# Optimization experiments

Hardware: AMD Instinct MI355X
Metric: run time of the kernel (lower is better)

The kernel has to match this reference:

```python
import jax, jax.numpy as jnp
import numpy as np

BETA = 0.4
EPS = 0.05
NUM_CLASSES = 5


def _model_single(xi, W1, b1, W2, b2):
    # xi: [C, L] single sample -> logits [num_classes]
    h = jnp.tanh(xi.reshape(-1) @ W1 + b1)
    return h @ W2 + b2


def setup_inputs() -> dict:
    key = jax.random.key(0)
    k1, k2, k3, k4 = jax.random.split(key, 4)
    B, C, L, H = 8192, 1, 2048, 1024
    x = jax.random.normal(k1, (B, C, L), dtype=jnp.float32)
    y = jax.random.randint(k2, (B,), 0, NUM_CLASSES)
    W1 = jax.random.normal(k3, (C * L, H), dtype=jnp.float32) * (1.0 / np.sqrt(C * L).astype(np.float32))
    b1 = jnp.zeros((H,), dtype=jnp.float32)
    W2 = jax.random.normal(k4, (H, NUM_CLASSES), dtype=jnp.float32) * (1.0 / np.sqrt(H).astype(np.float32))
    b2 = jnp.zeros((NUM_CLASSES,), dtype=jnp.float32)
    return {"x": x, "y": y, "W1": W1, "b1": b1, "W2": W2, "b2": b2}


def reference(x, y, W1, b1, W2, b2):
    B = x.shape[0]
    # batched model forward (same math the torch loop calls per-sample)
    logits = jnp.tanh(x.reshape(B, -1) @ W1 + b1) @ W2 + b2  # [B, num_classes]

    y_onehot = jax.nn.one_hot(y, NUM_CLASSES, dtype=logits.dtype)
    mse_loss = jnp.mean((logits - y_onehot) ** 2)

    idx = jnp.arange(B)
    z_y = logits[idx, y]  # [B]
    margins = jnp.maximum(1.0 - z_y[:, None] + logits, 0.0)
    margins = margins.at[idx, y].set(0.0)
    margin_loss = margins.sum() / B

    # per-sample L1 norm of d z_y / d x_i: one batched vmap(grad) instead of a python loop
    def z_of_x(xi, yi):
        return _model_single(xi, W1, b1, W2, b2)[yi]

    grads = jax.vmap(jax.grad(z_of_x), in_axes=(0, 0))(x, y)  # [B, C, L]
    w_l1 = jnp.sum(jnp.abs(grads), axis=(1, 2))  # [B]

    R = w_l1 * EPS / (jnp.abs(z_y) + 1e-8)
    nsr_loss = BETA * jnp.mean(jnp.log1p(R))

    correct_mask = jnp.mean((jnp.argmax(logits, axis=1) == y).astype(logits.dtype))
    total_loss = mse_loss + (margin_loss + nsr_loss) * correct_mask
    return total_loss
```

## Files before the change

### kernel.cpp

```cpp
#include <hip/hip_runtime.h>
#include <hip/hip_bf16.h>
#include <hip/hip_fp8.h>

typedef unsigned short ushort_t;
typedef unsigned char uchar_t;
typedef __attribute__((ext_vector_type(8))) short short8;
typedef __attribute__((ext_vector_type(8))) unsigned short u16x8;
typedef __attribute__((ext_vector_type(4))) float f32x4;

#define BETA 0.4f
#define EPS_C 0.05f
#define NB 8192
#define NH 1024
#define NL 2048
#define NC 5
#define VSCALE 64.0f

static __device__ __forceinline__ float b2f(unsigned short u) {
    union { unsigned int i; float f; } x; x.i = ((unsigned int)u) << 16; return x.f;
}
static __device__ __forceinline__ unsigned short f2b(float f) {
    union { float f; unsigned int i; } x; x.f = f;
    unsigned int i = x.i;
    unsigned int r = (i + 0x7FFFu + ((i >> 16) & 1u)) >> 16;
    return (unsigned short)r;
}
static __device__ __forceinline__ uchar_t f2fp8(float f) {
    __hip_fp8_e4m3 t(f);
    return (uchar_t)t.__x;
}

static __device__ __forceinline__ void gload16(const ushort_t* g, ushort_t* l) {
    __builtin_amdgcn_global_load_lds((const __attribute__((address_space(1))) void*)g,
                                     (__attribute__((address_space(3))) void*)l, 16, 0, 0);
}
static __device__ __forceinline__ void gload16b(const uchar_t* g, uchar_t* l) {
    __builtin_amdgcn_global_load_lds((const __attribute__((address_space(1))) void*)g,
                                     (__attribute__((address_space(3))) void*)l, 16, 0, 0);
}

#define CFENCE() asm volatile("" ::: "memory")
#define MFMA16(d, a, b) __builtin_amdgcn_mfma_f32_16x16x32_bf16(a, b, d, 0, 0, 0)
#define MFMA8(d, a, b)  __builtin_amdgcn_mfma_f32_16x16x32_fp8_fp8(a, b, d, 0, 0, 0)

__global__ __launch_bounds__(256) void cvt_kernel(const float* __restrict__ in,
                                                  ushort_t* __restrict__ out, long n) {
    long i = ((long)blockIdx.x * 256 + threadIdx.x) * 8;
    if (i >= n) return;
    const float4 a = *(const float4*)(in + i);
    const float4 b = *(const float4*)(in + i + 4);
    u16x8 o;
    o[0] = f2b(a.x); o[1] = f2b(a.y); o[2] = f2b(a.z); o[3] = f2b(a.w);
    o[4] = f2b(b.x); o[5] = f2b(b.y); o[6] = f2b(b.z); o[7] = f2b(b.w);
    *(u16x8*)(out + i) = o;
}

__global__ __launch_bounds__(256) void trans_kernel(const float* __restrict__ W1,
                                                    ushort_t* __restrict__ W1Tb,
                                                    uchar_t* __restrict__ W1f8) {
    __shared__ float tile[32][33];
    const int tx = threadIdx.x & 31, ty = threadIdx.x >> 5;
    const int k0 = blockIdx.x * 32, n0 = blockIdx.y * 32;
#pragma unroll
    for (int i = 0; i < 4; ++i) {
        const float v = W1[(size_t)(k0 + ty + i * 8) * NH + n0 + tx];
        tile[ty + i * 8][tx] = v;
        W1f8[(size_t)(k0 + ty + i * 8) * NH + n0 + tx] = f2fp8(v * VSCALE);
    }
    __syncthreads();
#pragma unroll
    for (int i = 0; i < 4; ++i)
        W1Tb[(size_t)(n0 + ty + i * 8) * NL + k0 + tx] = f2b(tile[tx][ty + i * 8]);
}

__global__ __launch_bounds__(256, 2) void g128_1(const ushort_t* __restrict__ A,
                                                 const ushort_t* __restrict__ Bt,
                                                 const float* __restrict__ b1,
                                                 ushort_t* __restrict__ hout) {
    constexpr int K  = 2048;
    constexpr int NT = K / 64;

    __shared__ ushort_t As[2][8192];
    __shared__ ushort_t Bs[2][8192];

    const int tid = threadIdx.x;
    const int wv = tid >> 6, lane = tid & 63;
    const int wm = (wv >> 1) & 1, wn = wv & 1;
    const int fr = lane & 15, fg = lane >> 4;

    const int xcd = blockIdx.x & 7, loc = blockIdx.x >> 3;
    const int bm0 = (xcd * 8 + (loc >> 3)) * 128;
    const int bn0 = (loc & 7) * 128;

    const int srow = lane >> 3;
    const int scol = ((lane & 7) ^ srow) << 3;

#define STA(BUF, KT) {                                                      \
    _Pragma("unroll") for (int c_ = 0; c_ < 4; ++c_) {                      \
        const int row_ = c_ * 32 + wv * 8 + srow;                           \
        gload16(A + (size_t)(bm0 + row_) * K + (KT) * 64 + scol,            \
                &As[BUF][c_ * 2048 + wv * 512]);                            \
    } }
#define STB(BUF, KT) {                                                      \
    _Pragma("unroll") for (int c_ = 0; c_ < 4; ++c_) {                      \
        const int row_ = c_ * 32 + wv * 8 + srow;                           \
        gload16(Bt + (size_t)(bn0 + row_) * K + (KT) * 64 + scol,           \
                &Bs[BUF][c_ * 2048 + wv * 512]);                            \
    } }

    auto ldA = [&](int buf, int mf, int ks) -> short8 {
        const int row = wm * 64 + mf * 16 + fr;
        const int slot = ((ks << 2) + fg) ^ (row & 7);
        return *(const short8*)&As[buf][row * 64 + slot * 8];
    };
    auto ldB = [&](int buf, int nf, int ks) -> short8 {
        const int row = wn * 64 + nf * 16 + fr;
        const int slot = ((ks << 2) + fg) ^ (row & 7);
        return *(const short8*)&Bs[buf][row * 64 + slot * 8];
    };

    f32x4 acc[4][4] = {};

    STA(0, 0) STB(0, 0)
    asm volatile("s_waitcnt vmcnt(0)" ::: "memory");
    CFENCE(); __builtin_amdgcn_s_barrier(); CFENCE();

#define TILE(BUF, TT) {                                                     \
    const int t_ = (TT);                                                    \
    short8 af[4][2], bf[4][2];                                              \
    _Pragma("unroll") for (int n_ = 0; n_ < 4; ++n_) {                      \
        bf[n_][0] = ldB(BUF, n_, 0); bf[n_][1] = ldB(BUF, n_, 1);           \
    }                                                                       \
    _Pragma("unroll") for (int m_ = 0; m_ < 4; ++m_) {                      \
        af[m_][0] = ldA(BUF, m_, 0); af[m_][1] = ldA(BUF, m_, 1);           \
    }                                                                       \
    if (t_ + 1 < NT) { STA(BUF ^ 1, t_ + 1) STB(BUF ^ 1, t_ + 1) }          \
    CFENCE(); __builtin_amdgcn_s_barrier(); CFENCE();                       \
    __builtin_amdgcn_s_setprio(1);                                          \
    _Pragma("unroll") for (int m_ = 0; m_ < 4; ++m_)                        \
        _Pragma("unroll") for (int n_ = 0; n_ < 4; ++n_) {                  \
            acc[m_][n_] = MFMA16(acc[m_][n_], af[m_][0], bf[n_][0]);        \
            acc[m_][n_] = MFMA16(acc[m_][n_], af[m_][1], bf[n_][1]);        \
        }                                                                   \
    __builtin_amdgcn_s_setprio(0);                                          \
    asm volatile("s_waitcnt vmcnt(0)" ::: "memory");                        \
    CFENCE(); __builtin_amdgcn_s_barrier(); CFENCE();                       \
    }

#pragma unroll 1
    for (int t = 0; t < NT; t += 2) {
        TILE(0, t)
        TILE(1, t + 1)
    }
#undef TILE
#undef STA
#undef STB

#pragma unroll
    for (int m = 0; m < 4; ++m)
#pragma unroll
        for (int n = 0; n < 4; ++n) {
            const int col = bn0 + wn * 64 + n * 16 + fr;
            const float bb = b1[col];
            const size_t rbase = (size_t)(bm0 + wm * 64 + m * 16 + fg * 4) * NH + col;
#pragma unroll
            for (int r = 0; r < 4; ++r)
                hout[rbase + (size_t)r * NH] = f2b(tanhf(acc[m][n][r] + bb));
        }
}

__global__ __launch_bounds__(256, 4) void g2f8(const uchar_t* __restrict__ A,
                                               const uchar_t* __restrict__ Bt,
                                               float* __restrict__ partout) {
    constexpr int K  = 1024;
    constexpr int NT = K / 64;

    __shared__ uchar_t As[2][8192];
    __shared__ uchar_t Bs[2][8192];

    const int tid = threadIdx.x;
    const int wv = tid >> 6, lane = tid & 63;
    const int wm = (wv >> 1) & 1, wn = wv & 1;
    const int fr = lane & 15, fg = lane >> 4;

    const int xcd = blockIdx.x & 7, loc = blockIdx.x >> 3;
    const int bm0 = (xcd * 8 + (loc >> 4)) * 128;
    const int bnIdx = loc & 15;
    const int bn0 = bnIdx * 128;

    const int t8 = tid >> 3, t7 = tid & 7;

#define STAF(BUF, KT) {                                                     \
    _Pragma("unroll") for (int j_ = 0; j_ < 2; ++j_) {                      \
        const int r1_ = j_ * 32 + t8;                                       \
        const int sl_ = (t7 * 2) ^ ((r1_ & 7) << 1);                        \
        const int row_ = 2 * r1_ + (sl_ >> 3);                              \
        const int cb_ = (KT) * 64 + (sl_ & 7) * 8;                          \
        gload16b(A + (size_t)(bm0 + row_) * K + cb_,                        \
                 &As[BUF][j_ * 4096 + wv * 1024]);                          \
    } }
#define STBF(BUF, KT) {                                                     \
    _Pragma("unroll") for (int j_ = 0; j_ < 2; ++j_) {                      \
        const int r1_ = j_ * 32 + t8;                                       \
        const int sl_ = (t7 * 2) ^ ((r1_ & 7) << 1);                        \
        const int row_ = 2 * r1_ + (sl_ >> 3);                              \
        const int cb_ = (KT) * 64 + (sl_ & 7) * 8;                          \
        gload16b(Bt + (size_t)(bn0 + row_) * K + cb_,                       \
                 &Bs[BUF][j_ * 4096 + wv * 1024]);                          \
    } }

    auto ldA = [&](int buf, int mf, int ks) -> long {
        const int row = wm * 64 + mf * 16 + fr;
        const int r1 = row >> 1;
        const int phys = (((row & 1) << 3) | (ks << 2) | fg) ^ ((r1 & 7) << 1);
        return *(const long*)&As[buf][r1 * 128 + phys * 8];
    };
    auto ldB = [&](int buf, int nf, int ks) -> long {
        const int row = wn * 64 + nf * 16 + fr;
        const int r1 = row >> 1;
        const int phys = (((row & 1) << 3) | (ks << 2) | fg) ^ ((r1 & 7) << 1);
        return *(const long*)&Bs[buf][r1 * 128 + phys * 8];
    };

    f32x4 acc[4][4] = {};

    STAF(0, 0) STBF(0, 0)
    asm volatile("s_waitcnt vmcnt(0)" ::: "memory");
    CFENCE(); __builtin_amdgcn_s_barrier(); CFENCE();

#define TILEF(BUF, TT) {                                                    \
    const int t_ = (TT);                                                    \
    long af[4][2], bf[4][2];                                                \
    _Pragma("unroll") for (int n_ = 0; n_ < 4; ++n_) {                      \
        bf[n_][0] = ldB(BUF, n_, 0); bf[n_][1] = ldB(BUF, n_, 1);           \
    }                                                                       \
    _Pragma("unroll") for (int m_ = 0; m_ < 4; ++m_) {                      \
        af[m_][0] = ldA(BUF, m_, 0); af[m_][1] = ldA(BUF, m_, 1);           \
    }                                                                       \
    if (t_ + 1 < NT) { STAF(BUF ^ 1, t_ + 1) STBF(BUF ^ 1, t_ + 1) }        \
    CFENCE(); __builtin_amdgcn_s_barrier(); CFENCE();                       \
    __builtin_amdgcn_s_setprio(1);                                          \
    _Pragma("unroll") for (int m_ = 0; m_ < 4; ++m_)                        \
        _Pragma("unroll") for (int n_ = 0; n_ < 4; ++n_) {                  \
            acc[m_][n_] = MFMA8(acc[m_][n_], af[m_][0], bf[n_][0]);         \
            acc[m_][n_] = MFMA8(acc[m_][n_], af[m_][1], bf[n_][1]);         \
        }                                                                   \
    __builtin_amdgcn_s_setprio(0);                                          \
    asm volatile("s_waitcnt vmcnt(0)" ::: "memory");                        \
    CFENCE(); __builtin_amdgcn_s_barrier(); CFENCE();                       \
    }

#pragma unroll 1
    for (int t = 0; t < NT; t += 2) {
        TILEF(0, t)
        TILEF(1, t + 1)
    }
#undef TILEF
#undef STAF
#undef STBF

    __syncthreads();
    float* rsum = (float*)&As[0][0];
#pragma unroll
    for (int m = 0; m < 4; ++m)
#pragma unroll
        for (int r = 0; r < 4; ++r) {
            float s = 0.f;
#pragma unroll
            for (int n = 0; n < 4; ++n) s += fabsf(acc[m][n][r]);
            s += __shfl_xor(s, 1); s += __shfl_xor(s, 2);
            s += __shfl_xor(s, 4); s += __shfl_xor(s, 8);
            if (fr == 0) rsum[wn * 128 + wm * 64 + m * 16 + fg * 4 + r] = s;
        }
    __syncthreads();
    if (tid < 128)
        partout[(size_t)bnIdx * NB + bm0 + tid] = rsum[tid] + rsum[128 + tid];
}

__global__ __launch_bounds__(256) void rows_kernel(const ushort_t* __restrict__ hb,
                                                   const int* __restrict__ y,
                                                   const float* __restrict__ W2,
                                                   const float* __restrict__ b2,
                                                   uchar_t* __restrict__ vb,
                                                   float4* __restrict__ rowstats) {
    __shared__ float w2t[NC][NH];
    __shared__ float b2s[NC];
    const int tid = threadIdx.x;
    for (int i = tid; i < NH * NC; i += 256) w2t[i % NC][i / NC] = W2[i];
    if (tid < NC) b2s[tid] = b2[tid];
    __syncthreads();
    const int wid = tid >> 6, lane = tid & 63;
    const int row = blockIdx.x * 4 + wid;
    const ushort_t* hrow = hb + (size_t)row * NH;
    uchar_t* vrow = vb + (size_t)row * NH;
    const int yi = y[row];
    float d0 = 0, d1 = 0, d2 = 0, d3 = 0, d4 = 0;
#pragma unroll
    for (int it = 0; it < 2; ++it) {
        const int n0 = it * 512 + lane * 8;
        u16x8 hv = *(const u16x8*)(hrow + n0);
        float hh[8];
#pragma unroll
        for (int j = 0; j < 8; ++j) hh[j] = b2f(hv[j]);
#pragma unroll
        for (int c = 0; c < NC; ++c) {
            const float4 a = *(const float4*)&w2t[c][n0];
            const float4 b = *(const float4*)&w2t[c][n0 + 4];
            float d = hh[0] * a.x; d += hh[1] * a.y; d += hh[2] * a.z; d += hh[3] * a.w;
            d += hh[4] * b.x; d += hh[5] * b.y; d += hh[6] * b.z; d += hh[7] * b.w;
            if (c == 0) d0 += d; else if (c == 1) d1 += d; else if (c == 2) d2 += d;
            else if (c == 3) d3 += d; else d4 += d;
        }
        const float4 ya = *(const float4*)&w2t[yi][n0];
        const float4 yb = *(const float4*)&w2t[yi][n0 + 4];
        const float yw[8] = { ya.x, ya.y, ya.z, ya.w, yb.x, yb.y, yb.z, yb.w };
        union { uchar_t b[8]; long l; } ov;
#pragma unroll
        for (int j = 0; j < 8; ++j)
            ov.b[j] = f2fp8((1.f - hh[j] * hh[j]) * yw[j] * VSCALE);
        *(long*)(vrow + n0) = ov.l;
    }
#pragma unroll
    for (int off = 32; off; off >>= 1) {
        d0 += __shfl_xor(d0, off); d1 += __shfl_xor(d1, off); d2 += __shfl_xor(d2, off);
        d3 += __shfl_xor(d3, off); d4 += __shfl_xor(d4, off);
    }
    if (lane == 0) {
        float lg[NC] = { d0 + b2s[0], d1 + b2s[1], d2 + b2s[2], d3 + b2s[3], d4 + b2s[4] };
        float zy = lg[yi];
        float mse = 0.f, marg = 0.f;
        int amax = 0; float best = lg[0];
#pragma unroll
        for (int c = 0; c < NC; ++c) {
            float t = lg[c] - (c == yi ? 1.f : 0.f);
            mse += t * t;
            if (c != yi) marg += fmaxf(1.f - zy + lg[c], 0.f);
            if (lg[c] > best) { best = lg[c]; amax = c; }
        }
        rowstats[row] = make_float4(zy, mse, marg, (amax == yi) ? 1.f : 0.f);
    }
}

__global__ __launch_bounds__(256) void reduce_rows(const float4* __restrict__ rs,
                                                   const float* __restrict__ part,
                                                   int NT, float4* __restrict__ bsums) {
    const int tid = threadIdx.x;
    const int r = blockIdx.x * 256 + tid;
    float4 v = rs[r];
    float wl1 = 0.f;
    for (int t = 0; t < NT; ++t) wl1 += part[(size_t)t * NB + r];
    wl1 *= (1.0f / (VSCALE * VSCALE));
    float R = wl1 * EPS_C / (fabsf(v.x) + 1e-8f);
    float4 s = make_float4(v.y, v.z, v.w, log1pf(R));
#pragma unroll
    for (int off = 32; off; off >>= 1) {
        s.x += __shfl_down(s.x, off); s.y += __shfl_down(s.y, off);
        s.z += __shfl_down(s.z, off); s.w += __shfl_down(s.w, off);
    }
    __shared__ float4 red[4];
    if ((tid & 63) == 0) red[tid >> 6] = s;
    __syncthreads();
    if (tid == 0) {
        float4 t = red[0];
        for (int i = 1; i < 4; ++i) { t.x += red[i].x; t.y += red[i].y; t.z += red[i].z; t.w += red[i].w; }
        bsums[blockIdx.x] = t;
    }
}

__global__ void final_combine(const float4* __restrict__ bsums, int nb, float* __restrict__ out) {
    const int l = threadIdx.x;
    float4 s = (l < nb) ? bsums[l] : make_float4(0.f, 0.f, 0.f, 0.f);
#pragma unroll
    for (int off = 32; off; off >>= 1) {
        s.x += __shfl_down(s.x, off); s.y += __shfl_down(s.y, off);
        s.z += __shfl_down(s.z, off); s.w += __shfl_down(s.w, off);
    }
    if (l == 0) {
        const float Bf = (float)NB;
        out[0] = s.x / (Bf * (float)NC) + (s.y / Bf + BETA * s.w / Bf) * (s.z / Bf);
    }
}

extern "C" void kernel_launch(void* const* d_in, const int* in_sizes, int n_in,
                              void* d_out, int out_size, void* d_ws, size_t ws_size,
                              hipStream_t stream) {
    const float* x  = (const float*)d_in[0];
    const int*   y  = (const int*)d_in[1];
    const float* W1 = (const float*)d_in[2];
    const float* b1 = (const float*)d_in[3];
    const float* W2 = (const float*)d_in[4];
    const float* b2 = (const float*)d_in[5];
    float* out = (float*)d_out;

    char* ws = (char*)d_ws;
    ushort_t* W1Tb = (ushort_t*)(ws);
    uchar_t*  W1f8 = (uchar_t*)(ws + (4ul << 20));
    ushort_t* xb   = (ushort_t*)(ws + (8ul << 20));
    ushort_t* hb   = (ushort_t*)(ws + (40ul << 20));
    uchar_t*  vf8  = (uchar_t*)(ws + (56ul << 20));
    float4*   rowstats = (float4*)(ws + (72ul << 20));
    float*    part = (float*)(ws + (72ul << 20) + (1ul << 20));
    float4*   bsums = (float4*)(ws + (74ul << 20));

    cvt_kernel<<<(NB * (long)NL) / (256 * 8), 256, 0, stream>>>(x, xb, (long)NB * NL);
    trans_kernel<<<dim3(NL / 32, NH / 32), 256, 0, stream>>>(W1, W1Tb, W1f8);

    g128_1<<<512, 256, 0, stream>>>(xb, W1Tb, b1, hb);

    rows_kernel<<<NB / 4, 256, 0, stream>>>(hb, y, W2, b2, vf8, rowstats);

    g2f8<<<1024, 256, 0, stream>>>(vf8, W1f8, part);

    reduce_rows<<<NB / 256, 256, 0, stream>>>(rowstats, part, NL / 128, bsums);
    final_combine<<<1, 64, 0, stream>>>(bsums, NB / 256, out);
}
```

Baseline: 113.0 us.

## Restructure first GEMM to two waves per block with 128x64 warp tiles

The bf16 x·W1 GEMM now runs 128-thread blocks (2 waves), each wave computing a full 128x64 output tile with 8x4 MFMA accumulators. The K step shrinks from 64 to 32, and the LDS layout packs two 32-wide rows per 64-element line with an XOR swizzle. The aim is more MFMA work per LDS fragment load and less shared memory per block. The cost is doubled accumulator registers, fewer waves per CU, and twice as many barrier iterations over K.

```diff
diff --git a/kernel.cpp b/kernel.cpp
--- a/kernel.cpp
+++ b/kernel.cpp
@@ -73,53 +73,60 @@
         W1Tb[(size_t)(n0 + ty + i * 8) * NL + k0 + tx] = f2b(tile[tx][ty + i * 8]);
 }
 
-__global__ __launch_bounds__(256, 2) void g128_1(const ushort_t* __restrict__ A,
-                                                 const ushort_t* __restrict__ Bt,
-                                                 const float* __restrict__ b1,
-                                                 ushort_t* __restrict__ hout) {
+__global__ __launch_bounds__(128, 2) void g128_2w(const ushort_t* __restrict__ A,
+                                                  const ushort_t* __restrict__ Bt,
+                                                  const float* __restrict__ b1,
+                                                  ushort_t* __restrict__ hout) {
     constexpr int K  = 2048;
-    constexpr int NT = K / 64;
-
-    __shared__ ushort_t As[2][8192];
-    __shared__ ushort_t Bs[2][8192];
+    constexpr int NT = K / 32;
+
+    __shared__ ushort_t As[2][4096];
+    __shared__ ushort_t Bs[2][4096];
 
     const int tid = threadIdx.x;
     const int wv = tid >> 6, lane = tid & 63;
-    const int wm = (wv >> 1) & 1, wn = wv & 1;
+    const int wn = wv;
     const int fr = lane & 15, fg = lane >> 4;
 
     const int xcd = blockIdx.x & 7, loc = blockIdx.x >> 3;
     const int bm0 = (xcd * 8 + (loc >> 3)) * 128;
     const int bn0 = (loc & 7) * 128;
 
-    const int srow = lane >> 3;
-    const int scol = ((lane & 7) ^ srow) << 3;
+    const int t8 = tid >> 3, t7 = tid & 7;
 
 #define STA(BUF, KT) {                                                      \
-    _Pragma("unroll") for (int c_ = 0; c_ < 4; ++c_) {                      \
-        const int row_ = c_ * 32 + wv * 8 + srow;                           \
-        gload16(A + (size_t)(bm0 + row_) * K + (KT) * 64 + scol,            \
-                &As[BUF][c_ * 2048 + wv * 512]);                            \
+    _Pragma("unroll") for (int j_ = 0; j_ < 4; ++j_) {                      \
+        const int r1_ = j_ * 16 + t8;                                       \
+        const int sl_ = t7 ^ (r1_ & 7);                                     \
+        const int row_ = 2 * r1_ + (sl_ >> 2);                              \
+        const int col_ = (KT) * 32 + (sl_ & 3) * 8;                         \
+        gload16(A + (size_t)(bm0 + row_) * K + col_,                        \
+                &As[BUF][j_ * 1024 + wv * 512]);                            \
     } }
 #define STB(BUF, KT) {                                                      \
-    _Pragma("unroll") for (int c_ = 0; c_ < 4; ++c_) {                      \
-        const int row_ = c_ * 32 + wv * 8 + srow;                           \
-        gload16(Bt + (size_t)(bn0 + row_) * K + (KT) * 64 + scol,           \
-                &Bs[BUF][c_ * 2048 + wv * 512]);                            \
+    _Pragma("unroll") for (int j_ = 0; j_ < 4; ++j_) {                      \
+        const int r1_ = j_ * 16 + t8;                                       \
+        const int sl_ = t7 ^ (r1_ & 7);                                     \
+        const int row_ = 2 * r1_ + (sl_ >> 2);                              \
+        const int col_ = (KT) * 32 + (sl_ & 3) * 8;                         \
+        gload16(Bt + (size_t)(bn0 + row_) * K + col_,                       \
+                &Bs[BUF][j_ * 1024 + wv * 512]);                            \
     } }
 
-    auto ldA = [&](int buf, int mf, int ks) -> short8 {
-        const int row = wm * 64 + mf * 16 + fr;
-        const int slot = ((ks << 2) + fg) ^ (row & 7);
-        return *(const short8*)&As[buf][row * 64 + slot * 8];
+    auto ldA = [&](int buf, int mf) -> short8 {
+        const int row = mf * 16 + fr;
+        const int r1 = row >> 1;
+        const int phys = ((((row & 1) << 2) | fg) ^ (r1 & 7));
+        return *(const short8*)&As[buf][r1 * 64 + phys * 8];
     };
-    auto ldB = [&](int buf, int nf, int ks) -> short8 {
+    auto ldB = [&](int buf, int nf) -> short8 {
         const int row = wn * 64 + nf * 16 + fr;
-        const int slot = ((ks << 2) + fg) ^ (row & 7);
-        return *(const short8*)&Bs[buf][row * 64 + slot * 8];
+        const int r1 = row >> 1;
+        const int phys = ((((row & 1) << 2) | fg) ^ (r1 & 7));
+        return *(const short8*)&Bs[buf][r1 * 64 + phys * 8];
     };
 
-    f32x4 acc[4][4] = {};
+    f32x4 acc[8][4] = {};
 
     STA(0, 0) STB(0, 0)
     asm volatile("s_waitcnt vmcnt(0)" ::: "memory");
@@ -127,21 +134,15 @@
 
 #define TILE(BUF, TT) {                                                     \
     const int t_ = (TT);                                                    \
-    short8 af[4][2], bf[4][2];                                              \
-    _Pragma("unroll") for (int n_ = 0; n_ < 4; ++n_) {                      \
-        bf[n_][0] = ldB(BUF, n_, 0); bf[n_][1] = ldB(BUF, n_, 1);           \
-    }                                                                       \
-    _Pragma("unroll") for (int m_ = 0; m_ < 4; ++m_) {                      \
-        af[m_][0] = ldA(BUF, m_, 0); af[m_][1] = ldA(BUF, m_, 1);           \
-    }                                                                       \
+    short8 af[8], bf[4];                                                    \
+    _Pragma("unroll") for (int n_ = 0; n_ < 4; ++n_) bf[n_] = ldB(BUF, n_); \
+    _Pragma("unroll") for (int m_ = 0; m_ < 8; ++m_) af[m_] = ldA(BUF, m_); \
     if (t_ + 1 < NT) { STA(BUF ^ 1, t_ + 1) STB(BUF ^ 1, t_ + 1) }          \
     CFENCE(); __builtin_amdgcn_s_barrier(); CFENCE();                       \
     __builtin_amdgcn_s_setprio(1);                                          \
-    _Pragma("unroll") for (int m_ = 0; m_ < 4; ++m_)                        \
-        _Pragma("unroll") for (int n_ = 0; n_ < 4; ++n_) {                  \
-            acc[m_][n_] = MFMA16(acc[m_][n_], af[m_][0], bf[n_][0]);        \
-            acc[m_][n_] = MFMA16(acc[m_][n_], af[m_][1], bf[n_][1]);        \
-        }                                                                   \
+    _Pragma("unroll") for (int m_ = 0; m_ < 8; ++m_)                        \
+        _Pragma("unroll") for (int n_ = 0; n_ < 4; ++n_)                    \
+            acc[m_][n_] = MFMA16(acc[m_][n_], af[m_], bf[n_]);              \
     __builtin_amdgcn_s_setprio(0);                                          \
     asm volatile("s_waitcnt vmcnt(0)" ::: "memory");                        \
     CFENCE(); __builtin_amdgcn_s_barrier(); CFENCE();                       \
@@ -157,12 +158,12 @@
 #undef STB
 
 #pragma unroll
-    for (int m = 0; m < 4; ++m)
+    for (int m = 0; m < 8; ++m)
 #pragma unroll
         for (int n = 0; n < 4; ++n) {
             const int col = bn0 + wn * 64 + n * 16 + fr;
             const float bb = b1[col];
-            const size_t rbase = (size_t)(bm0 + wm * 64 + m * 16 + fg * 4) * NH + col;
+            const size_t rbase = (size_t)(bm0 + m * 16 + fg * 4) * NH + col;
 #pragma unroll
             for (int r = 0; r < 4; ++r)
                 hout[rbase + (size_t)r * NH] = f2b(tanhf(acc[m][n][r] + bb));
@@ -405,7 +406,7 @@
     cvt_kernel<<<(NB * (long)NL) / (256 * 8), 256, 0, stream>>>(x, xb, (long)NB * NL);
     trans_kernel<<<dim3(NL / 32, NH / 32), 256, 0, stream>>>(W1, W1Tb, W1f8);
 
-    g128_1<<<512, 256, 0, stream>>>(xb, W1Tb, b1, hb);
+    g128_2w<<<512, 128, 0, stream>>>(xb, W1Tb, b1, hb);
 
     rows_kernel<<<NB / 4, 256, 0, stream>>>(hb, y, W2, b2, vf8, rowstats);
 
```

Measured after the change: 134.4 us. 18.9% more time.
